# Performance work log

Hardware: AMD Instinct MI355X
Metric: run time of the kernel (lower is better)

## Reference

```python
import jax, jax.numpy as jnp
import numpy as np

D_MODEL = 1024
NUM_HEADS = 16
HEAD_DIM = D_MODEL // NUM_HEADS
B, S = 2, 2048


def setup_inputs() -> dict:
    key = jax.random.key(0)
    ks = jax.random.split(key, 8)
    scale = 1.0 / np.sqrt(D_MODEL)
    inp = {
        "query": jax.random.normal(ks[0], (B, S, D_MODEL), jnp.float32),
        "key": jax.random.normal(ks[1], (B, S, D_MODEL), jnp.float32),
        "value": jax.random.normal(ks[2], (B, S, D_MODEL), jnp.float32),
        # causal mask, broadcastable over batch and heads
        "mask": jnp.tril(jnp.ones((S, S), dtype=bool))[None, None, :, :],
        # torch nn.Linear weights: y = x @ W.T (+ b)
        "Wq": jax.random.normal(ks[3], (D_MODEL, D_MODEL), jnp.float32) * scale,
        "Wk": jax.random.normal(ks[4], (D_MODEL, D_MODEL), jnp.float32) * scale,
        "Wv": jax.random.normal(ks[5], (D_MODEL, D_MODEL), jnp.float32) * scale,
        "Wo": jax.random.normal(ks[6], (D_MODEL, D_MODEL), jnp.float32) * scale,
        "bo": jax.random.normal(ks[7], (D_MODEL,), jnp.float32) * scale,
    }
    return inp


def _split_heads(x):
    b, s, _ = x.shape
    return x.reshape(b, s, NUM_HEADS, HEAD_DIM).transpose(0, 2, 1, 3)  # [B,H,S,Dh]


def reference(query, key, value, mask, Wq, Wk, Wv, Wo, bo):
    q = _split_heads(query @ Wq.T)
    k = _split_heads(key @ Wk.T)
    v = _split_heads(value @ Wv.T)
    scores = jnp.einsum("bhqd,bhkd->bhqk", q, k) / jnp.sqrt(jnp.float32(HEAD_DIM))
    scores = jnp.where(mask, scores, jnp.float32(-jnp.inf))
    attn = jax.nn.softmax(scores, axis=-1)
    out = jnp.einsum("bhqk,bhkd->bhqd", attn, v)  # [B,H,S,Dh]
    out = out.transpose(0, 2, 1, 3).reshape(query.shape[0], q.shape[2], D_MODEL)
    return out @ Wo.T + bo
```

## Files before the change

kernel.cpp:

```cpp
#include <hip/hip_runtime.h>
#include <hip/hip_bf16.h>

#define DM   1024
#define NH   16
#define HD   64
#define SEQ  2048
#define BATCH 2
#define MTOT (BATCH*SEQ)

typedef unsigned short u16;
typedef __attribute__((ext_vector_type(8))) short bf16x8;
typedef __attribute__((ext_vector_type(4))) float f32x4;

#define SC2F 0.1803368801111464f

__device__ __forceinline__ float bf2f(u16 h) {
  union { unsigned int i; float f; } u; u.i = ((unsigned int)h) << 16; return u.f;
}
__device__ __forceinline__ u16 f2bf(float f) {
  union { float f; unsigned int i; } u; u.f = f;
  unsigned int r = u.i + 0x7fffu + ((u.i >> 16) & 1u);
  return (u16)(r >> 16);
}
__device__ __forceinline__ unsigned int pk2(float lo, float hi) {
  union { float f; unsigned int u; } a, b; a.f = lo; b.f = hi;
  return ((a.u + 0x8000u) >> 16) | ((b.u + 0x8000u) & 0xFFFF0000u);
}
__device__ __forceinline__ unsigned int cvtpk(float lo, float hi) {
  unsigned int r;
  asm("v_cvt_pk_bf16_f32 %0, %1, %2" : "=v"(r) : "v"(lo), "v"(hi));
  return r;
}

__device__ __forceinline__ uint4 load8_bf16(const void* base, size_t elemOff, bool isf32) {
  if (!isf32) return *(const uint4*)((const u16*)base + elemOff);
  const float* f = (const float*)base + elemOff;
  f32x4 a = *(const f32x4*)f;
  f32x4 b = *(const f32x4*)(f + 4);
  union { u16 h[8]; uint4 v; } r;
  r.h[0]=f2bf(a[0]); r.h[1]=f2bf(a[1]); r.h[2]=f2bf(a[2]); r.h[3]=f2bf(a[3]);
  r.h[4]=f2bf(b[0]); r.h[5]=f2bf(b[1]); r.h[6]=f2bf(b[2]); r.h[7]=f2bf(b[3]);
  return r.v;
}

__global__ __launch_bounds__(256) void prep(
    const void* __restrict__ q, const void* __restrict__ k, const void* __restrict__ v,
    const void* __restrict__ wq, const void* __restrict__ wk, const void* __restrict__ wv,
    const void* __restrict__ wo, const void* __restrict__ bo,
    u16* __restrict__ Xq, u16* __restrict__ Xk, u16* __restrict__ Xv,
    u16* __restrict__ Wqb, u16* __restrict__ Wkb, u16* __restrict__ Wvb, u16* __restrict__ Wob,
    float* __restrict__ biasf, int* __restrict__ flag_out)
{
  const int tid = threadIdx.x;
  __shared__ int cnts[4];
  {
    const u16* qs = (const u16*)q;
    int e0 = (qs[tid*2]   >> 7) & 0xFF;
    int e1 = (qs[tid*2+1] >> 7) & 0xFF;
    int c = ((e0 >= 0x6E && e0 <= 0x8F) ? 1 : 0) + ((e1 >= 0x6E && e1 <= 0x8F) ? 1 : 0);
    c += __shfl_xor(c, 1);  c += __shfl_xor(c, 2);  c += __shfl_xor(c, 4);
    c += __shfl_xor(c, 8);  c += __shfl_xor(c, 16); c += __shfl_xor(c, 32);
    if ((tid & 63) == 0) cnts[tid >> 6] = c;
  }
  __syncthreads();
  const bool isf32 = (cnts[0] + cnts[1] + cnts[2] + cnts[3]) < 400;

  const int z = blockIdx.z;
  if (z == 7) {
    if (blockIdx.x == 0) {
      if (tid == 0) *flag_out = isf32 ? 0 : 1;
      for (int i = tid; i < DM; i += 256)
        biasf[i] = isf32 ? ((const float*)bo)[i] : bf2f(((const u16*)bo)[i]);
    }
    return;
  }
  const void* src; u16* dst; size_t n;
  switch (z) {
    case 0: src=q;  dst=Xq;  n=(size_t)MTOT*DM; break;
    case 1: src=k;  dst=Xk;  n=(size_t)MTOT*DM; break;
    case 2: src=v;  dst=Xv;  n=(size_t)MTOT*DM; break;
    case 3: src=wq; dst=Wqb; n=(size_t)DM*DM;   break;
    case 4: src=wk; dst=Wkb; n=(size_t)DM*DM;   break;
    case 5: src=wv; dst=Wvb; n=(size_t)DM*DM;   break;
    default: src=wo; dst=Wob; n=(size_t)DM*DM;  break;
  }
  const size_t stride = (size_t)gridDim.x * 256 * 8;
  for (size_t i = ((size_t)blockIdx.x * 256 + tid) * 8; i < n; i += stride)
    *(uint4*)(dst + i) = load8_bf16(src, i, isf32);
}

__device__ __forceinline__ void gld16(const u16* g, u16* l) {
  __builtin_amdgcn_global_load_lds(
      (const __attribute__((address_space(1))) void*)g,
      (__attribute__((address_space(3))) void*)l, 16, 0, 0);
}

__global__ __launch_bounds__(256) void gemm_qkv(
    const u16* __restrict__ X0, const u16* __restrict__ X1, const u16* __restrict__ X2,
    const u16* __restrict__ W0, const u16* __restrict__ W1, const u16* __restrict__ W2,
    u16* __restrict__ F0, u16* __restrict__ F1, u16* __restrict__ F2)
{
  __shared__ __align__(16) u16 smem[24576];
  u16* const A0 = smem;
  u16* const A1 = smem + 4096;
  u16* const A2 = smem + 8192;
  u16* const B0 = smem + 12288;
  u16* const B1 = smem + 16384;
  u16* const B2 = smem + 20480;

  const int zz = blockIdx.z;
  const u16* X = (zz==0) ? X0 : ((zz==1) ? X1 : X2);
  const u16* W = (zz==0) ? W0 : ((zz==1) ? W1 : W2);
  u16* outF    = (zz==0) ? F0 : ((zz==1) ? F1 : F2);

  const int tid = threadIdx.x;
  const int wave = tid >> 6, lane = tid & 63, quad = lane >> 4, l16 = lane & 15;
  const int wr = wave >> 1, wc = wave & 1;
  const int m0 = blockIdx.x * 128, n0 = blockIdx.y * 128;

  const int sg = ((lane & 3) ^ ((lane >> 3) & 3)) * 8;
  const int rS = wave*32 + (lane >> 2);
  const u16* gA0 = X + (size_t)(m0 + rS)*DM + sg;
  const u16* gA1 = X + (size_t)(m0 + rS + 16)*DM + sg;
  const u16* gB0 = W + (size_t)(n0 + rS)*DM + sg;
  const u16* gB1 = W + (size_t)(n0 + rS + 16)*DM + sg;
  const int so = wave*1024;

  const int xslot8 = (quad ^ ((l16 >> 1) & 3)) * 8;

  f32x4 acc[4][4];
#pragma unroll
  for (int i = 0; i < 4; i++)
#pragma unroll
    for (int j = 0; j < 4; j++) { acc[i][j][0]=0.f; acc[i][j][1]=0.f; acc[i][j][2]=0.f; acc[i][j][3]=0.f; }

  gld16(gA0, A0 + so);
  gld16(gA1, A0 + so + 512);
  gld16(gB0, B0 + so);
  gld16(gB1, B0 + so + 512);
  asm volatile("" ::: "memory");

  int cur = 0;
  for (int k0 = 0; k0 < DM; k0 += 32) {
    u16* const Ab = (cur == 0) ? A0 : ((cur == 1) ? A1 : A2);
    u16* const Bb = (cur == 0) ? B0 : ((cur == 1) ? B1 : B2);
    const int nxt = (cur == 2) ? 0 : cur + 1;
    if (k0 + 32 < DM) {
      u16* const An = (nxt == 0) ? A0 : ((nxt == 1) ? A1 : A2);
      u16* const Bn = (nxt == 0) ? B0 : ((nxt == 1) ? B1 : B2);
      gld16(gA0 + k0 + 32, An + so);
      gld16(gA1 + k0 + 32, An + so + 512);
      gld16(gB0 + k0 + 32, Bn + so);
      gld16(gB1 + k0 + 32, Bn + so + 512);
      asm volatile("s_waitcnt vmcnt(4)" ::: "memory");
    } else {
      asm volatile("s_waitcnt vmcnt(0)" ::: "memory");
    }
    __builtin_amdgcn_s_barrier();
    asm volatile("" ::: "memory");

    bf16x8 af[4], bfr[4];
#pragma unroll
    for (int fr = 0; fr < 4; fr++)
      af[fr] = *(const bf16x8*)&Ab[(wr*64 + fr*16 + l16)*32 + xslot8];
#pragma unroll
    for (int fc = 0; fc < 4; fc++)
      bfr[fc] = *(const bf16x8*)&Bb[(wc*64 + fc*16 + l16)*32 + xslot8];
#pragma unroll
    for (int fr = 0; fr < 4; fr++)
#pragma unroll
      for (int fc = 0; fc < 4; fc++)
        acc[fr][fc] = __builtin_amdgcn_mfma_f32_16x16x32_bf16(af[fr], bfr[fc], acc[fr][fc], 0, 0, 0);

    asm volatile("" ::: "memory");
    cur = nxt;
  }

  if (zz == 2) {
    u16* const Ts = smem;
    const int bb = m0 >> 11;
    const int s0 = m0 & (SEQ-1);
#pragma unroll
    for (int p = 0; p < 2; p++) {
      __syncthreads();
      if (wc == p) {
#pragma unroll
        for (int fr = 0; fr < 4; fr++) {
#pragma unroll
          for (int fc = 0; fc < 4; fc++) {
            const int dl = fc*16 + l16;
            const int sb = wr*64 + fr*16 + quad*4;
            const int slot = (sb >> 3) ^ (dl & 15);
            u16* rowp = &Ts[dl*128 + slot*8 + (sb & 7)];
            *(unsigned int*)(rowp)     = pk2(acc[fr][fc][0], acc[fr][fc][1]);
            *(unsigned int*)(rowp + 2) = pk2(acc[fr][fc][2], acc[fr][fc][3]);
          }
        }
      }
      __syncthreads();
      const int dl2 = tid >> 2, ch4 = tid & 3;
      const int hh = (n0 + p*64) >> 6;
      u16* dst = outF + ((size_t)(bb*NH + hh)*HD + dl2)*SEQ + s0 + ch4*32;
#pragma unroll
      for (int j = 0; j < 4; j++) {
        const int c  = ch4*4 + j;
        const int lo = (c >> 2)*32 + (c & 3)*4;
        const int hi = lo + 16;
        uint2 lo2 = *(const uint2*)&Ts[dl2*128 + (((lo >> 3) ^ (dl2 & 15))*8) + (lo & 7)];
        uint2 hi2 = *(const uint2*)&Ts[dl2*128 + (((hi >> 3) ^ (dl2 & 15))*8) + (hi & 7)];
        uint4 o; o.x = lo2.x; o.y = lo2.y; o.z = hi2.x; o.w = hi2.y;
        *(uint4*)&dst[j*8] = o;
      }
    }
    return;
  }

#pragma unroll
  for (int fr = 0; fr < 4; fr++) {
#pragma unroll
    for (int rr = 0; rr < 4; rr++) {
      const int m = m0 + wr*64 + fr*16 + quad*4 + rr;
#pragma unroll
      for (int fc = 0; fc < 4; fc++) {
        const int n = n0 + wc*64 + fc*16 + l16;
        float vv = acc[fr][fc][rr];
        if (zz == 0) vv *= SC2F;
        const int b = m >> 11, s = m & (SEQ-1), h = n >> 6, d = n & (HD-1);
        outF[((size_t)(b*NH + h)*SEQ + s)*HD + d] = f2bf(vv);
      }
    }
  }
}

__global__ __launch_bounds__(256) void gemm_out(
    const u16* __restrict__ X, const u16* __restrict__ W,
    const float* __restrict__ biasf, void* __restrict__ outP,
    const int* __restrict__ dflag)
{
  __shared__ __align__(16) u16 smem[18432];
  u16* const A0 = smem;
  u16* const A1 = smem + 4096;
  u16* const A2 = smem + 8192;
  u16* const B0 = smem + 12288;
  u16* const B1 = smem + 14336;
  u16* const B2 = smem + 16384;

  const int tid = threadIdx.x;
  const int wave = tid >> 6, lane = tid & 63, quad = lane >> 4, l16 = lane & 15;
  const int wr = wave >> 1, wc = wave & 1;
  const int m0 = blockIdx.x * 128, n0 = blockIdx.y * 64;

  const int sg = ((lane & 3) ^ ((lane >> 3) & 3)) * 8;
  const int rA = wave*32 + (lane >> 2);
  const int rB = wave*16 + (lane >> 2);
  const u16* gA0 = X + (size_t)(m0 + rA)*DM + sg;
  const u16* gA1 = X + (size_t)(m0 + rA + 16)*DM + sg;
  const u16* gB0 = W + (size_t)(n0 + rB)*DM + sg;
  const int soA = wave*1024, soB = wave*512;

  const int xslot8 = (quad ^ ((l16 >> 1) & 3)) * 8;

  f32x4 acc[4][2];
#pragma unroll
  for (int i = 0; i < 4; i++)
#pragma unroll
    for (int j = 0; j < 2; j++) { acc[i][j][0]=0.f; acc[i][j][1]=0.f; acc[i][j][2]=0.f; acc[i][j][3]=0.f; }

  gld16(gA0, A0 + soA);
  gld16(gA1, A0 + soA + 512);
  gld16(gB0, B0 + soB);
  asm volatile("" ::: "memory");

  int cur = 0;
  for (int k0 = 0; k0 < DM; k0 += 32) {
    u16* const Ab = (cur == 0) ? A0 : ((cur == 1) ? A1 : A2);
    u16* const Bb = (cur == 0) ? B0 : ((cur == 1) ? B1 : B2);
    const int nxt = (cur == 2) ? 0 : cur + 1;
    if (k0 + 32 < DM) {
      u16* const An = (nxt == 0) ? A0 : ((nxt == 1) ? A1 : A2);
      u16* const Bn = (nxt == 0) ? B0 : ((nxt == 1) ? B1 : B2);
      gld16(gA0 + k0 + 32, An + soA);
      gld16(gA1 + k0 + 32, An + soA + 512);
      gld16(gB0 + k0 + 32, Bn + soB);
      asm volatile("s_waitcnt vmcnt(3)" ::: "memory");
    } else {
      asm volatile("s_waitcnt vmcnt(0)" ::: "memory");
    }
    __builtin_amdgcn_s_barrier();
    asm volatile("" ::: "memory");

    bf16x8 af[4], bfr[2];
#pragma unroll
    for (int fr = 0; fr < 4; fr++)
      af[fr] = *(const bf16x8*)&Ab[(wr*64 + fr*16 + l16)*32 + xslot8];
#pragma unroll
    for (int fc = 0; fc < 2; fc++)
      bfr[fc] = *(const bf16x8*)&Bb[(wc*32 + fc*16 + l16)*32 + xslot8];
#pragma unroll
    for (int fr = 0; fr < 4; fr++)
#pragma unroll
      for (int fc = 0; fc < 2; fc++)
        acc[fr][fc] = __builtin_amdgcn_mfma_f32_16x16x32_bf16(af[fr], bfr[fc], acc[fr][fc], 0, 0, 0);

    asm volatile("" ::: "memory");
    cur = nxt;
  }

  const bool isf32 = (*dflag == 0);
#pragma unroll
  for (int fr = 0; fr < 4; fr++) {
#pragma unroll
    for (int rr = 0; rr < 4; rr++) {
      const int m = m0 + wr*64 + fr*16 + quad*4 + rr;
#pragma unroll
      for (int fc = 0; fc < 2; fc++) {
        const int n = n0 + wc*32 + fc*16 + l16;
        float vv = acc[fr][fc][rr] + biasf[n];
        if (isf32) ((float*)outP)[(size_t)m*DM + n] = vv;
        else       ((u16*)outP)[(size_t)m*DM + n]   = f2bf(vv);
      }
    }
  }
}

__global__ __launch_bounds__(256) void attn_mfma(
    const u16* __restrict__ Qb, const u16* __restrict__ Kb,
    const u16* __restrict__ Vtb,
    u16* __restrict__ aO)
{
  __shared__ u16 Ks[2][64*64];
  __shared__ u16 Vs[2][64*64];

  const int bh = blockIdx.x;
  const int py = blockIdx.y;
  int qt;
  if      (py < 8)  qt = 31 - py;
  else if (py < 16) qt = py - 8;
  else if (py < 24) qt = 39 - py;
  else              qt = py - 16;

  const u16* Qp = Qb  + (size_t)bh * SEQ * HD;
  const u16* Kp = Kb  + (size_t)bh * SEQ * HD;
  const u16* Vp = Vtb + (size_t)bh * HD * SEQ;

  const int tid  = threadIdx.x;
  const int wave = tid >> 6, lane = tid & 63, quad = lane >> 4, l16 = lane & 15;

  const int i0 = wave*128 + lane, i1 = i0 + 64;
  const int r0 = i0 >> 3, c0 = (i0 & 7) ^ (r0 & 7);
  const int r1 = i1 >> 3, c1 = (i1 & 7) ^ (r1 & 7);
  const int kq_off0 = r0*HD + c0*8;
  const int kq_off1 = r1*HD + c1*8;
  const int v_off0  = r0*SEQ + c0*8;
  const int v_off1  = r1*SEQ + c1*8;

  const int l7 = l16 & 7;
  const int ql = wave*16 + l16;
  const int so = wave*1024;

  const int khi = qt + 1;
  const int qg = qt*64 + ql;

  const u16* qrow = Qp + (size_t)qg * HD;
  const bf16x8 bq0 = *(const bf16x8*)(qrow + quad*8);
  const bf16x8 bq1 = *(const bf16x8*)(qrow + 32 + quad*8);

  f32x4 O[4];
#pragma unroll
  for (int u = 0; u < 4; u++) { O[u][0]=0.f; O[u][1]=0.f; O[u][2]=0.f; O[u][3]=0.f; }
  float mi = -__builtin_inff();
  f32x4 lv = {0.f, 0.f, 0.f, 0.f};

  gld16(Kp + kq_off0, &Ks[0][so]);
  gld16(Kp + kq_off1, &Ks[0][so + 512]);
  gld16(Vp + v_off0, &Vs[0][so]);
  gld16(Vp + v_off1, &Vs[0][so + 512]);
  asm volatile("" ::: "memory");

  for (int kt = 0; kt < khi; kt++) {
    const int cb = kt & 1;
    const u16* kb = &Ks[cb][0];
    const u16* vb = &Vs[cb][0];
    if (kt + 1 < khi) {
      u16* kn = &Ks[cb ^ 1][so];
      u16* vn = &Vs[cb ^ 1][so];
      gld16(Kp + (kt+1)*(64*HD) + kq_off0, kn);
      gld16(Kp + (kt+1)*(64*HD) + kq_off1, kn + 512);
      gld16(Vp + (kt+1)*64 + v_off0, vn);
      gld16(Vp + (kt+1)*64 + v_off1, vn + 512);
      asm volatile("s_waitcnt vmcnt(4)" ::: "memory");
    } else {
      asm volatile("s_waitcnt vmcnt(0)" ::: "memory");
    }
    __builtin_amdgcn_s_barrier();
    asm volatile("" ::: "memory");

    f32x4 st[4];
#pragma unroll
    for (int t = 0; t < 4; t++) { st[t][0]=0.f; st[t][1]=0.f; st[t][2]=0.f; st[t][3]=0.f; }
#pragma unroll
    for (int s = 0; s < 2; s++) {
      const bf16x8 bq = s ? bq1 : bq0;
      const int ch = s*4 + quad;
#pragma unroll
      for (int t = 0; t < 4; t++) {
        bf16x8 ak = *(const bf16x8*)&kb[((t*16 + l16)*8 + (ch ^ l7))*8];
        st[t] = __builtin_amdgcn_mfma_f32_16x16x32_bf16(ak, bq, st[t], 0, 0, 0);
      }
    }

    if (kt == qt) {
#pragma unroll
      for (int t = 0; t < 4; t++)
#pragma unroll
        for (int r = 0; r < 4; r++)
          if (kt*64 + t*16 + quad*4 + r > qg) st[t][r] = -__builtin_inff();
    }

    f32x4 m01 = __builtin_elementwise_max(st[0], st[1]);
    f32x4 m23 = __builtin_elementwise_max(st[2], st[3]);
    f32x4 mm  = __builtin_elementwise_max(m01, m23);
    float mx = fmaxf(fmaxf(mm[0], mm[1]), fmaxf(mm[2], mm[3]));
    mx = fmaxf(mx, __shfl_xor(mx, 16));
    mx = fmaxf(mx, __shfl_xor(mx, 32));

    if (__any(mx > mi + 8.0f)) {
      const float nm = fmaxf(mi, mx);
      const float al = exp2f(mi - nm);
      mi = nm;
      const f32x4 alv = {al, al, al, al};
      lv *= alv;
      O[0] *= alv; O[1] *= alv; O[2] *= alv; O[3] *= alv;
    }

    const f32x4 miv = {mi, mi, mi, mi};
    unsigned int w[4][2];
    f32x4 e0, e1, e2, e3;
    {
      f32x4 d0 = st[0] - miv, d1 = st[1] - miv, d2 = st[2] - miv, d3 = st[3] - miv;
      e0[0]=exp2f(d0[0]); e0[1]=exp2f(d0[1]); e0[2]=exp2f(d0[2]); e0[3]=exp2f(d0[3]);
      e1[0]=exp2f(d1[0]); e1[1]=exp2f(d1[1]); e1[2]=exp2f(d1[2]); e1[3]=exp2f(d1[3]);
      e2[0]=exp2f(d2[0]); e2[1]=exp2f(d2[1]); e2[2]=exp2f(d2[2]); e2[3]=exp2f(d2[3]);
      e3[0]=exp2f(d3[0]); e3[1]=exp2f(d3[1]); e3[2]=exp2f(d3[2]); e3[3]=exp2f(d3[3]);
    }
    w[0][0] = cvtpk(e0[0], e0[1]); w[0][1] = cvtpk(e0[2], e0[3]);
    w[1][0] = cvtpk(e1[0], e1[1]); w[1][1] = cvtpk(e1[2], e1[3]);
    w[2][0] = cvtpk(e2[0], e2[1]); w[2][1] = cvtpk(e2[2], e2[3]);
    w[3][0] = cvtpk(e3[0], e3[1]); w[3][1] = cvtpk(e3[2], e3[3]);
    lv += (e0 + e1) + (e2 + e3);

#pragma unroll
    for (int s = 0; s < 2; s++) {
      union { unsigned int u[4]; bf16x8 v; } bp;
      bp.u[0] = w[2*s][0];   bp.u[1] = w[2*s][1];
      bp.u[2] = w[2*s+1][0]; bp.u[3] = w[2*s+1][1];
      const int ch = s*4 + quad;
#pragma unroll
      for (int u = 0; u < 4; u++) {
        bf16x8 av = *(const bf16x8*)&vb[((u*16 + l16)*8 + (ch ^ l7))*8];
        O[u] = __builtin_amdgcn_mfma_f32_16x16x32_bf16(av, bp.v, O[u], 0, 0, 0);
      }
    }

    asm volatile("" ::: "memory");
    __builtin_amdgcn_s_barrier();
    asm volatile("" ::: "memory");
  }

  float ls = (lv[0] + lv[1]) + (lv[2] + lv[3]);
  ls += __shfl_xor(ls, 16);
  ls += __shfl_xor(ls, 32);
  const float inv = 1.0f / ls;

  const int b = bh >> 4, h = bh & 15;
  u16* outp = aO + ((size_t)(b*SEQ + qt*64 + ql))*DM + h*HD;
#pragma unroll
  for (int u = 0; u < 4; u++) {
    uint2 u2;
    u2.x = pk2(O[u][0]*inv, O[u][1]*inv);
    u2.y = pk2(O[u][2]*inv, O[u][3]*inv);
    *(uint2*)&outp[u*16 + quad*4] = u2;
  }
}

extern "C" void kernel_launch(void* const* d_in, const int* in_sizes, int n_in,
                              void* d_out, int out_size, void* d_ws, size_t ws_size,
                              hipStream_t stream) {
  const void* q  = d_in[0];
  const void* k  = d_in[1];
  const void* v  = d_in[2];
  const void* wq = d_in[4];
  const void* wk = d_in[5];
  const void* wv = d_in[6];
  const void* wo = d_in[7];
  const void* bo = d_in[8];

  const size_t TX = (size_t)MTOT*DM;
  const size_t TW = (size_t)DM*DM;
  u16* ws  = (u16*)d_ws;
  u16* Xq  = ws;
  u16* Xk  = ws + TX;
  u16* Xv  = ws + 2*TX;
  u16* Wqb = ws + 3*TX;
  u16* Wkb = Wqb + TW;
  u16* Wvb = Wqb + 2*TW;
  u16* Wob = Wqb + 3*TW;
  u16* Qw  = ws + 3*TX + 4*TW;
  u16* Kw  = Qw + TX;
  u16* Vt  = Qw + 2*TX;
  u16*   aO     = Xq;
  float* biasf  = (float*)(Qw + 3*TX);
  int*   fl     = (int*)(biasf + DM);

  dim3 blk(256);
  prep<<<dim3(512, 1, 8), blk, 0, stream>>>(q, k, v, wq, wk, wv, wo, bo,
      Xq, Xk, Xv, Wqb, Wkb, Wvb, Wob, biasf, fl);
  gemm_qkv<<<dim3(MTOT/128, DM/128, 3), blk, 0, stream>>>(
      Xq, Xk, Xv, Wqb, Wkb, Wvb, Qw, Kw, Vt);
  attn_mfma<<<dim3(BATCH*NH, 32, 1), blk, 0, stream>>>(Qw, Kw, Vt, aO);
  gemm_out<<<dim3(MTOT/128, DM/64), blk, 0, stream>>>(aO, Wob, biasf, d_out, fl);
}
```

Measured before the change: 224.9 us.

## Fuse fp32-to-bf16 conversion into GEMM loads, drop separate prep conversion pass

The prep kernel no longer converts the activations and weights to bf16 in a workspace. Instead, the QKV and output GEMMs load fp32 (or bf16) directly from global memory into registers, convert them with v_cvt_pk_bf16_f32, and store the result to LDS in a register-staged double buffer. This replaces the earlier triple-buffered async global_load_lds pipeline. It removes a full read-write pass over roughly 50MB of inputs, at the cost of more VGPRs and a shallower prefetch depth in the GEMMs. In gemm_out only the weight operand is staged through registers.

```diff
diff --git a/kernel.cpp b/kernel.cpp
--- a/kernel.cpp
+++ b/kernel.cpp
@@ -31,24 +31,15 @@
   asm("v_cvt_pk_bf16_f32 %0, %1, %2" : "=v"(r) : "v"(lo), "v"(hi));
   return r;
 }
-
-__device__ __forceinline__ uint4 load8_bf16(const void* base, size_t elemOff, bool isf32) {
-  if (!isf32) return *(const uint4*)((const u16*)base + elemOff);
-  const float* f = (const float*)base + elemOff;
-  f32x4 a = *(const f32x4*)f;
-  f32x4 b = *(const f32x4*)(f + 4);
-  union { u16 h[8]; uint4 v; } r;
-  r.h[0]=f2bf(a[0]); r.h[1]=f2bf(a[1]); r.h[2]=f2bf(a[2]); r.h[3]=f2bf(a[3]);
-  r.h[4]=f2bf(b[0]); r.h[5]=f2bf(b[1]); r.h[6]=f2bf(b[2]); r.h[7]=f2bf(b[3]);
-  return r.v;
+__device__ __forceinline__ uint4 cvt8(const f32x4& a, const f32x4& b) {
+  uint4 r;
+  r.x = cvtpk(a[0], a[1]); r.y = cvtpk(a[2], a[3]);
+  r.z = cvtpk(b[0], b[1]); r.w = cvtpk(b[2], b[3]);
+  return r;
 }
 
 __global__ __launch_bounds__(256) void prep(
-    const void* __restrict__ q, const void* __restrict__ k, const void* __restrict__ v,
-    const void* __restrict__ wq, const void* __restrict__ wk, const void* __restrict__ wv,
-    const void* __restrict__ wo, const void* __restrict__ bo,
-    u16* __restrict__ Xq, u16* __restrict__ Xk, u16* __restrict__ Xv,
-    u16* __restrict__ Wqb, u16* __restrict__ Wkb, u16* __restrict__ Wvb, u16* __restrict__ Wob,
+    const void* __restrict__ q, const void* __restrict__ bo,
     float* __restrict__ biasf, int* __restrict__ flag_out)
 {
   const int tid = threadIdx.x;
@@ -64,29 +55,9 @@
   }
   __syncthreads();
   const bool isf32 = (cnts[0] + cnts[1] + cnts[2] + cnts[3]) < 400;
-
-  const int z = blockIdx.z;
-  if (z == 7) {
-    if (blockIdx.x == 0) {
-      if (tid == 0) *flag_out = isf32 ? 0 : 1;
-      for (int i = tid; i < DM; i += 256)
-        biasf[i] = isf32 ? ((const float*)bo)[i] : bf2f(((const u16*)bo)[i]);
-    }
-    return;
-  }
-  const void* src; u16* dst; size_t n;
-  switch (z) {
-    case 0: src=q;  dst=Xq;  n=(size_t)MTOT*DM; break;
-    case 1: src=k;  dst=Xk;  n=(size_t)MTOT*DM; break;
-    case 2: src=v;  dst=Xv;  n=(size_t)MTOT*DM; break;
-    case 3: src=wq; dst=Wqb; n=(size_t)DM*DM;   break;
-    case 4: src=wk; dst=Wkb; n=(size_t)DM*DM;   break;
-    case 5: src=wv; dst=Wvb; n=(size_t)DM*DM;   break;
-    default: src=wo; dst=Wob; n=(size_t)DM*DM;  break;
-  }
-  const size_t stride = (size_t)gridDim.x * 256 * 8;
-  for (size_t i = ((size_t)blockIdx.x * 256 + tid) * 8; i < n; i += stride)
-    *(uint4*)(dst + i) = load8_bf16(src, i, isf32);
+  if (tid == 0) *flag_out = isf32 ? 0 : 1;
+  for (int i = tid; i < DM; i += 256)
+    biasf[i] = isf32 ? ((const float*)bo)[i] : bf2f(((const u16*)bo)[i]);
 }
 
 __device__ __forceinline__ void gld16(const u16* g, u16* l) {
@@ -96,22 +67,23 @@
 }
 
 __global__ __launch_bounds__(256) void gemm_qkv(
-    const u16* __restrict__ X0, const u16* __restrict__ X1, const u16* __restrict__ X2,
-    const u16* __restrict__ W0, const u16* __restrict__ W1, const u16* __restrict__ W2,
-    u16* __restrict__ F0, u16* __restrict__ F1, u16* __restrict__ F2)
+    const void* __restrict__ X0, const void* __restrict__ X1, const void* __restrict__ X2,
+    const void* __restrict__ W0, const void* __restrict__ W1, const void* __restrict__ W2,
+    u16* __restrict__ F0, u16* __restrict__ F1, u16* __restrict__ F2,
+    const int* __restrict__ dflag)
 {
-  __shared__ __align__(16) u16 smem[24576];
+  __shared__ __align__(16) u16 smem[16384];
   u16* const A0 = smem;
   u16* const A1 = smem + 4096;
-  u16* const A2 = smem + 8192;
-  u16* const B0 = smem + 12288;
-  u16* const B1 = smem + 16384;
-  u16* const B2 = smem + 20480;
+  u16* const B0 = smem + 8192;
+  u16* const B1 = smem + 12288;
 
   const int zz = blockIdx.z;
-  const u16* X = (zz==0) ? X0 : ((zz==1) ? X1 : X2);
-  const u16* W = (zz==0) ? W0 : ((zz==1) ? W1 : W2);
-  u16* outF    = (zz==0) ? F0 : ((zz==1) ? F1 : F2);
+  const void* X = (zz==0) ? X0 : ((zz==1) ? X1 : X2);
+  const void* W = (zz==0) ? W0 : ((zz==1) ? W1 : W2);
+  u16* outF     = (zz==0) ? F0 : ((zz==1) ? F1 : F2);
+
+  const bool isf32 = (*dflag == 0);
 
   const int tid = threadIdx.x;
   const int wave = tid >> 6, lane = tid & 63, quad = lane >> 4, l16 = lane & 15;
@@ -120,11 +92,11 @@
 
   const int sg = ((lane & 3) ^ ((lane >> 3) & 3)) * 8;
   const int rS = wave*32 + (lane >> 2);
-  const u16* gA0 = X + (size_t)(m0 + rS)*DM + sg;
-  const u16* gA1 = X + (size_t)(m0 + rS + 16)*DM + sg;
-  const u16* gB0 = W + (size_t)(n0 + rS)*DM + sg;
-  const u16* gB1 = W + (size_t)(n0 + rS + 16)*DM + sg;
-  const int so = wave*1024;
+  const size_t offA0 = (size_t)(m0 + rS)*DM + sg;
+  const size_t offA1 = offA0 + (size_t)16*DM;
+  const size_t offB0 = (size_t)(n0 + rS)*DM + sg;
+  const size_t offB1 = offB0 + (size_t)16*DM;
+  const int wsl = wave*1024 + lane*8;
 
   const int xslot8 = (quad ^ ((l16 >> 1) & 3)) * 8;
 
@@ -134,47 +106,77 @@
 #pragma unroll
     for (int j = 0; j < 4; j++) { acc[i][j][0]=0.f; acc[i][j][1]=0.f; acc[i][j][2]=0.f; acc[i][j][3]=0.f; }
 
-  gld16(gA0, A0 + so);
-  gld16(gA1, A0 + so + 512);
-  gld16(gB0, B0 + so);
-  gld16(gB1, B0 + so + 512);
+  f32x4 fA0a, fA0b, fA1a, fA1b, fB0a, fB0b, fB1a, fB1b;
+  uint4 hA0, hA1, hB0, hB1;
+
+#define LD8(base, off)                                             \
+  if (isf32) { const float* fp = (const float*)(base) + (off);     \
+    f_a = *(const f32x4*)fp; f_b = *(const f32x4*)(fp + 4); }      \
+  else h_ = *(const uint4*)((const u16*)(base) + (off));
+
+  {
+#define LDI(base, off, fa, fb, hh) { f32x4 f_a, f_b; uint4 h_;     \
+    LD8(base, off); fa = f_a; fb = f_b; hh = h_; }
+    LDI(X, offA0, fA0a, fA0b, hA0)
+    LDI(X, offA1, fA1a, fA1b, hA1)
+    LDI(W, offB0, fB0a, fB0b, hB0)
+    LDI(W, offB1, fB1a, fB1b, hB1)
+    uint4 wA0 = isf32 ? cvt8(fA0a, fA0b) : hA0;
+    uint4 wA1 = isf32 ? cvt8(fA1a, fA1b) : hA1;
+    uint4 wB0 = isf32 ? cvt8(fB0a, fB0b) : hB0;
+    uint4 wB1 = isf32 ? cvt8(fB1a, fB1b) : hB1;
+    *(uint4*)&A0[wsl]       = wA0;
+    *(uint4*)&A0[wsl + 512] = wA1;
+    *(uint4*)&B0[wsl]       = wB0;
+    *(uint4*)&B0[wsl + 512] = wB1;
+  }
+  asm volatile("s_waitcnt lgkmcnt(0)" ::: "memory");
+  __builtin_amdgcn_s_barrier();
   asm volatile("" ::: "memory");
 
   int cur = 0;
   for (int k0 = 0; k0 < DM; k0 += 32) {
-    u16* const Ab = (cur == 0) ? A0 : ((cur == 1) ? A1 : A2);
-    u16* const Bb = (cur == 0) ? B0 : ((cur == 1) ? B1 : B2);
-    const int nxt = (cur == 2) ? 0 : cur + 1;
-    if (k0 + 32 < DM) {
-      u16* const An = (nxt == 0) ? A0 : ((nxt == 1) ? A1 : A2);
-      u16* const Bn = (nxt == 0) ? B0 : ((nxt == 1) ? B1 : B2);
-      gld16(gA0 + k0 + 32, An + so);
-      gld16(gA1 + k0 + 32, An + so + 512);
-      gld16(gB0 + k0 + 32, Bn + so);
-      gld16(gB1 + k0 + 32, Bn + so + 512);
-      asm volatile("s_waitcnt vmcnt(4)" ::: "memory");
-    } else {
-      asm volatile("s_waitcnt vmcnt(0)" ::: "memory");
+    const bool more = (k0 + 32 < DM);
+    if (more) {
+      LDI(X, offA0 + k0 + 32, fA0a, fA0b, hA0)
+      LDI(X, offA1 + k0 + 32, fA1a, fA1b, hA1)
+      LDI(W, offB0 + k0 + 32, fB0a, fB0b, hB0)
+      LDI(W, offB1 + k0 + 32, fB1a, fB1b, hB1)
+    }
+
+    u16* const Ab = cur ? A1 : A0;
+    u16* const Bb = cur ? B1 : B0;
+    bf16x8 af[4], bfr[4];
+#pragma unroll
+    for (int fr = 0; fr < 4; fr++)
+      af[fr] = *(const bf16x8*)&Ab[(wr*64 + fr*16 + l16)*32 + xslot8];
+#pragma unroll
+    for (int fc = 0; fc < 4; fc++)
+      bfr[fc] = *(const bf16x8*)&Bb[(wc*64 + fc*16 + l16)*32 + xslot8];
+#pragma unroll
+    for (int fr = 0; fr < 4; fr++)
+#pragma unroll
+      for (int fc = 0; fc < 4; fc++)
+        acc[fr][fc] = __builtin_amdgcn_mfma_f32_16x16x32_bf16(af[fr], bfr[fc], acc[fr][fc], 0, 0, 0);
+
+    if (more) {
+      u16* const An = cur ? A0 : A1;
+      u16* const Bn = cur ? B0 : B1;
+      uint4 wA0 = isf32 ? cvt8(fA0a, fA0b) : hA0;
+      uint4 wA1 = isf32 ? cvt8(fA1a, fA1b) : hA1;
+      uint4 wB0 = isf32 ? cvt8(fB0a, fB0b) : hB0;
+      uint4 wB1 = isf32 ? cvt8(fB1a, fB1b) : hB1;
+      *(uint4*)&An[wsl]       = wA0;
+      *(uint4*)&An[wsl + 512] = wA1;
+      *(uint4*)&Bn[wsl]       = wB0;
+      *(uint4*)&Bn[wsl + 512] = wB1;
+      asm volatile("s_waitcnt lgkmcnt(0)" ::: "memory");
     }
     __builtin_amdgcn_s_barrier();
     asm volatile("" ::: "memory");
-
-    bf16x8 af[4], bfr[4];
-#pragma unroll
-    for (int fr = 0; fr < 4; fr++)
-      af[fr] = *(const bf16x8*)&Ab[(wr*64 + fr*16 + l16)*32 + xslot8];
-#pragma unroll
-    for (int fc = 0; fc < 4; fc++)
-      bfr[fc] = *(const bf16x8*)&Bb[(wc*64 + fc*16 + l16)*32 + xslot8];
-#pragma unroll
-    for (int fr = 0; fr < 4; fr++)
-#pragma unroll
-      for (int fc = 0; fc < 4; fc++)
-        acc[fr][fc] = __builtin_amdgcn_mfma_f32_16x16x32_bf16(af[fr], bfr[fc], acc[fr][fc], 0, 0, 0);
-
-    asm volatile("" ::: "memory");
-    cur = nxt;
-  }
+    cur ^= 1;
+  }
+#undef LDI
 
   if (zz == 2) {
     u16* const Ts = smem;
@@ -233,17 +235,17 @@
 }
 
 __global__ __launch_bounds__(256) void gemm_out(
-    const u16* __restrict__ X, const u16* __restrict__ W,
+    const u16* __restrict__ X, const void* __restrict__ W,
     const float* __restrict__ biasf, void* __restrict__ outP,
     const int* __restrict__ dflag)
 {
-  __shared__ __align__(16) u16 smem[18432];
+  __shared__ __align__(16) u16 smem[12288];
   u16* const A0 = smem;
   u16* const A1 = smem + 4096;
-  u16* const A2 = smem + 8192;
-  u16* const B0 = smem + 12288;
-  u16* const B1 = smem + 14336;
-  u16* const B2 = smem + 16384;
+  u16* const B0 = smem + 8192;
+  u16* const B1 = smem + 10240;
+
+  const bool isf32 = (*dflag == 0);
 
   const int tid = threadIdx.x;
   const int wave = tid >> 6, lane = tid & 63, quad = lane >> 4, l16 = lane & 15;
@@ -255,8 +257,9 @@
   const int rB = wave*16 + (lane >> 2);
   const u16* gA0 = X + (size_t)(m0 + rA)*DM + sg;
   const u16* gA1 = X + (size_t)(m0 + rA + 16)*DM + sg;
-  const u16* gB0 = W + (size_t)(n0 + rB)*DM + sg;
-  const int soA = wave*1024, soB = wave*512;
+  const size_t offB = (size_t)(n0 + rB)*DM + sg;
+  const int soA = wave*1024;
+  const int wslB = wave*512 + lane*8;
 
   const int xslot8 = (quad ^ ((l16 >> 1) & 3)) * 8;
 
@@ -265,48 +268,61 @@
   for (int i = 0; i < 4; i++)
 #pragma unroll
     for (int j = 0; j < 2; j++) { acc[i][j][0]=0.f; acc[i][j][1]=0.f; acc[i][j][2]=0.f; acc[i][j][3]=0.f; }
+
+  f32x4 fBa, fBb; uint4 hB;
 
   gld16(gA0, A0 + soA);
   gld16(gA1, A0 + soA + 512);
-  gld16(gB0, B0 + soB);
+  { f32x4 f_a, f_b; uint4 h_;
+    LD8(W, offB)
+    fBa = f_a; fBb = f_b; hB = h_; }
+  {
+    uint4 wB = isf32 ? cvt8(fBa, fBb) : hB;
+    *(uint4*)&B0[wslB] = wB;
+  }
+  asm volatile("s_waitcnt vmcnt(0) lgkmcnt(0)" ::: "memory");
+  __builtin_amdgcn_s_barrier();
   asm volatile("" ::: "memory");
 
   int cur = 0;
   for (int k0 = 0; k0 < DM; k0 += 32) {
-    u16* const Ab = (cur == 0) ? A0 : ((cur == 1) ? A1 : A2);
-    u16* const Bb = (cur == 0) ? B0 : ((cur == 1) ? B1 : B2);
-    const int nxt = (cur == 2) ? 0 : cur + 1;
-    if (k0 + 32 < DM) {
-      u16* const An = (nxt == 0) ? A0 : ((nxt == 1) ? A1 : A2);
-      u16* const Bn = (nxt == 0) ? B0 : ((nxt == 1) ? B1 : B2);
+    const bool more = (k0 + 32 < DM);
+    if (more) {
+      u16* const An = cur ? A0 : A1;
       gld16(gA0 + k0 + 32, An + soA);
       gld16(gA1 + k0 + 32, An + soA + 512);
-      gld16(gB0 + k0 + 32, Bn + soB);
-      asm volatile("s_waitcnt vmcnt(3)" ::: "memory");
-    } else {
-      asm volatile("s_waitcnt vmcnt(0)" ::: "memory");
-    }
+      { f32x4 f_a, f_b; uint4 h_;
+        LD8(W, offB + k0 + 32)
+        fBa = f_a; fBb = f_b; hB = h_; }
+    }
+
+    u16* const Ab = cur ? A1 : A0;
+    u16* const Bb = cur ? B1 : B0;
+    bf16x8 af[4], bfr[2];
+#pragma unroll
+    for (int fr = 0; fr < 4; fr++)
+      af[fr] = *(const bf16x8*)&Ab[(wr*64 + fr*16 + l16)*32 + xslot8];
+#pragma unroll
+    for (int fc = 0; fc < 2; fc++)
+      bfr[fc] = *(const bf16x8*)&Bb[(wc*32 + fc*16 + l16)*32 + xslot8];
+#pragma unroll
+    for (int fr = 0; fr < 4; fr++)
+#pragma unroll
+      for (int fc = 0; fc < 2; fc++)
+        acc[fr][fc] = __builtin_amdgcn_mfma_f32_16x16x32_bf16(af[fr], bfr[fc], acc[fr][fc], 0, 0, 0);
+
+    if (more) {
+      u16* const Bn = cur ? B0 : B1;
+      uint4 wB = isf32 ? cvt8(fBa, fBb) : hB;
+      *(uint4*)&Bn[wslB] = wB;
+    }
+    asm volatile("s_waitcnt vmcnt(0) lgkmcnt(0)" ::: "memory");
     __builtin_amdgcn_s_barrier();
     asm volatile("" ::: "memory");
-
-    bf16x8 af[4], bfr[2];
-#pragma unroll
-    for (int fr = 0; fr < 4; fr++)
-      af[fr] = *(const bf16x8*)&Ab[(wr*64 + fr*16 + l16)*32 + xslot8];
-#pragma unroll
-    for (int fc = 0; fc < 2; fc++)
-      bfr[fc] = *(const bf16x8*)&Bb[(wc*32 + fc*16 + l16)*32 + xslot8];
-#pragma unroll
-    for (int fr = 0; fr < 4; fr++)
-#pragma unroll
-      for (int fc = 0; fc < 2; fc++)
-        acc[fr][fc] = __builtin_amdgcn_mfma_f32_16x16x32_bf16(af[fr], bfr[fc], acc[fr][fc], 0, 0, 0);
-
-    asm volatile("" ::: "memory");
-    cur = nxt;
-  }
-
-  const bool isf32 = (*dflag == 0);
+    cur ^= 1;
+  }
+
+  const bool isf32o = isf32;
 #pragma unroll
   for (int fr = 0; fr < 4; fr++) {
 #pragma unroll
@@ -316,8 +332,8 @@
       for (int fc = 0; fc < 2; fc++) {
         const int n = n0 + wc*32 + fc*16 + l16;
         float vv = acc[fr][fc][rr] + biasf[n];
-        if (isf32) ((float*)outP)[(size_t)m*DM + n] = vv;
-        else       ((u16*)outP)[(size_t)m*DM + n]   = f2bf(vv);
+        if (isf32o) ((float*)outP)[(size_t)m*DM + n] = vv;
+        else        ((u16*)outP)[(size_t)m*DM + n]   = f2bf(vv);
       }
     }
   }
@@ -496,27 +512,18 @@
   const void* bo = d_in[8];
 
   const size_t TX = (size_t)MTOT*DM;
-  const size_t TW = (size_t)DM*DM;
   u16* ws  = (u16*)d_ws;
-  u16* Xq  = ws;
-  u16* Xk  = ws + TX;
-  u16* Xv  = ws + 2*TX;
-  u16* Wqb = ws + 3*TX;
-  u16* Wkb = Wqb + TW;
-  u16* Wvb = Wqb + 2*TW;
-  u16* Wob = Wqb + 3*TW;
-  u16* Qw  = ws + 3*TX + 4*TW;
-  u16* Kw  = Qw + TX;
-  u16* Vt  = Qw + 2*TX;
-  u16*   aO     = Xq;
-  float* biasf  = (float*)(Qw + 3*TX);
-  int*   fl     = (int*)(biasf + DM);
+  u16* aO  = ws;
+  u16* Qw  = ws + TX;
+  u16* Kw  = ws + 2*TX;
+  u16* Vt  = ws + 3*TX;
+  float* biasf = (float*)(ws + 4*TX);
+  int*   fl    = (int*)(biasf + DM);
 
   dim3 blk(256);
-  prep<<<dim3(512, 1, 8), blk, 0, stream>>>(q, k, v, wq, wk, wv, wo, bo,
-      Xq, Xk, Xv, Wqb, Wkb, Wvb, Wob, biasf, fl);
+  prep<<<dim3(1), blk, 0, stream>>>(q, bo, biasf, fl);
   gemm_qkv<<<dim3(MTOT/128, DM/128, 3), blk, 0, stream>>>(
-      Xq, Xk, Xv, Wqb, Wkb, Wvb, Qw, Kw, Vt);
+      q, k, v, wq, wk, wv, Qw, Kw, Vt, fl);
   attn_mfma<<<dim3(BATCH*NH, 32, 1), blk, 0, stream>>>(Qw, Kw, Vt, aO);
-  gemm_out<<<dim3(MTOT/128, DM/64), blk, 0, stream>>>(aO, Wob, biasf, d_out, fl);
-}
+  gemm_out<<<dim3(MTOT/128, DM/64), blk, 0, stream>>>(aO, wo, biasf, d_out, fl);
+}
```

New measurement: 312.0 us. 1.39x slower.

## Fuse fp32-to-bf16 activation conversion into QKV GEMM A-tile loads

Applied to the files above, without the earlier changes.

The prep kernel no longer converts the three large q/k/v activation tensors to bf16. The QKV GEMM now reads the raw inputs through registers, converts them with v_cvt_pk_bf16_f32 and writes them to LDS, with the pipeline changed from three to two LDS buffers. This removes a full read and write pass over the activations, at the cost of register-staged A loads that can no longer use direct global-to-LDS copies. Conversion is repeated for each N tile, and the rounding differs slightly from the old f2bf.

```diff
diff --git a/kernel.cpp b/kernel.cpp
--- a/kernel.cpp
+++ b/kernel.cpp
@@ -29,6 +29,12 @@
 __device__ __forceinline__ unsigned int cvtpk(float lo, float hi) {
   unsigned int r;
   asm("v_cvt_pk_bf16_f32 %0, %1, %2" : "=v"(r) : "v"(lo), "v"(hi));
+  return r;
+}
+__device__ __forceinline__ uint4 cvt8(const f32x4& a, const f32x4& b) {
+  uint4 r;
+  r.x = cvtpk(a[0], a[1]); r.y = cvtpk(a[2], a[3]);
+  r.z = cvtpk(b[0], b[1]); r.w = cvtpk(b[2], b[3]);
   return r;
 }
 
@@ -44,11 +50,12 @@
 }
 
 __global__ __launch_bounds__(256) void prep(
-    const void* __restrict__ q, const void* __restrict__ k, const void* __restrict__ v,
-    const void* __restrict__ wq, const void* __restrict__ wk, const void* __restrict__ wv,
-    const void* __restrict__ wo, const void* __restrict__ bo,
-    u16* __restrict__ Xq, u16* __restrict__ Xk, u16* __restrict__ Xv,
-    u16* __restrict__ Wqb, u16* __restrict__ Wkb, u16* __restrict__ Wvb, u16* __restrict__ Wob,
+    const void* __restrict__ q,
+    const void* __restrict__ wq, const void* __restrict__ wk,
+    const void* __restrict__ wv, const void* __restrict__ wo,
+    const void* __restrict__ bo,
+    u16* __restrict__ Wqb, u16* __restrict__ Wkb,
+    u16* __restrict__ Wvb, u16* __restrict__ Wob,
     float* __restrict__ biasf, int* __restrict__ flag_out)
 {
   const int tid = threadIdx.x;
@@ -66,7 +73,7 @@
   const bool isf32 = (cnts[0] + cnts[1] + cnts[2] + cnts[3]) < 400;
 
   const int z = blockIdx.z;
-  if (z == 7) {
+  if (z == 4) {
     if (blockIdx.x == 0) {
       if (tid == 0) *flag_out = isf32 ? 0 : 1;
       for (int i = tid; i < DM; i += 256)
@@ -74,16 +81,9 @@
     }
     return;
   }
-  const void* src; u16* dst; size_t n;
-  switch (z) {
-    case 0: src=q;  dst=Xq;  n=(size_t)MTOT*DM; break;
-    case 1: src=k;  dst=Xk;  n=(size_t)MTOT*DM; break;
-    case 2: src=v;  dst=Xv;  n=(size_t)MTOT*DM; break;
-    case 3: src=wq; dst=Wqb; n=(size_t)DM*DM;   break;
-    case 4: src=wk; dst=Wkb; n=(size_t)DM*DM;   break;
-    case 5: src=wv; dst=Wvb; n=(size_t)DM*DM;   break;
-    default: src=wo; dst=Wob; n=(size_t)DM*DM;  break;
-  }
+  const void* src = (z==0) ? wq : (z==1) ? wk : (z==2) ? wv : wo;
+  u16* dst        = (z==0) ? Wqb : (z==1) ? Wkb : (z==2) ? Wvb : Wob;
+  const size_t n = (size_t)DM*DM;
   const size_t stride = (size_t)gridDim.x * 256 * 8;
   for (size_t i = ((size_t)blockIdx.x * 256 + tid) * 8; i < n; i += stride)
     *(uint4*)(dst + i) = load8_bf16(src, i, isf32);
@@ -96,22 +96,23 @@
 }
 
 __global__ __launch_bounds__(256) void gemm_qkv(
-    const u16* __restrict__ X0, const u16* __restrict__ X1, const u16* __restrict__ X2,
+    const void* __restrict__ X0, const void* __restrict__ X1, const void* __restrict__ X2,
     const u16* __restrict__ W0, const u16* __restrict__ W1, const u16* __restrict__ W2,
-    u16* __restrict__ F0, u16* __restrict__ F1, u16* __restrict__ F2)
+    u16* __restrict__ F0, u16* __restrict__ F1, u16* __restrict__ F2,
+    const int* __restrict__ dflag)
 {
-  __shared__ __align__(16) u16 smem[24576];
+  __shared__ __align__(16) u16 smem[16384];
   u16* const A0 = smem;
   u16* const A1 = smem + 4096;
-  u16* const A2 = smem + 8192;
-  u16* const B0 = smem + 12288;
-  u16* const B1 = smem + 16384;
-  u16* const B2 = smem + 20480;
+  u16* const B0 = smem + 8192;
+  u16* const B1 = smem + 12288;
 
   const int zz = blockIdx.z;
-  const u16* X = (zz==0) ? X0 : ((zz==1) ? X1 : X2);
-  const u16* W = (zz==0) ? W0 : ((zz==1) ? W1 : W2);
-  u16* outF    = (zz==0) ? F0 : ((zz==1) ? F1 : F2);
+  const void* X = (zz==0) ? X0 : ((zz==1) ? X1 : X2);
+  const u16* W  = (zz==0) ? W0 : ((zz==1) ? W1 : W2);
+  u16* outF     = (zz==0) ? F0 : ((zz==1) ? F1 : F2);
+
+  const bool isf32 = (*dflag == 0);
 
   const int tid = threadIdx.x;
   const int wave = tid >> 6, lane = tid & 63, quad = lane >> 4, l16 = lane & 15;
@@ -120,11 +121,12 @@
 
   const int sg = ((lane & 3) ^ ((lane >> 3) & 3)) * 8;
   const int rS = wave*32 + (lane >> 2);
-  const u16* gA0 = X + (size_t)(m0 + rS)*DM + sg;
-  const u16* gA1 = X + (size_t)(m0 + rS + 16)*DM + sg;
+  const size_t offA0 = (size_t)(m0 + rS)*DM + sg;
+  const size_t offA1 = offA0 + (size_t)16*DM;
   const u16* gB0 = W + (size_t)(n0 + rS)*DM + sg;
-  const u16* gB1 = W + (size_t)(n0 + rS + 16)*DM + sg;
-  const int so = wave*1024;
+  const u16* gB1 = gB0 + (size_t)16*DM;
+  const int so  = wave*1024;
+  const int wsl = wave*1024 + lane*8;
 
   const int xslot8 = (quad ^ ((l16 >> 1) & 3)) * 8;
 
@@ -134,29 +136,48 @@
 #pragma unroll
     for (int j = 0; j < 4; j++) { acc[i][j][0]=0.f; acc[i][j][1]=0.f; acc[i][j][2]=0.f; acc[i][j][3]=0.f; }
 
-  gld16(gA0, A0 + so);
-  gld16(gA1, A0 + so + 512);
+  f32x4 fa0, fb0, fa1, fb1; uint4 ha0, ha1;
+
+#define LDA(koff)                                                   \
+  if (isf32) {                                                      \
+    const float* p0 = (const float*)X + offA0 + (koff);             \
+    fa0 = *(const f32x4*)p0; fb0 = *(const f32x4*)(p0 + 4);         \
+    const float* p1 = (const float*)X + offA1 + (koff);             \
+    fa1 = *(const f32x4*)p1; fb1 = *(const f32x4*)(p1 + 4);         \
+  } else {                                                          \
+    ha0 = *(const uint4*)((const u16*)X + offA0 + (koff));          \
+    ha1 = *(const uint4*)((const u16*)X + offA1 + (koff));          \
+  }
+#define WRA(buf) {                                                  \
+    uint4 w0 = isf32 ? cvt8(fa0, fb0) : ha0;                        \
+    uint4 w1 = isf32 ? cvt8(fa1, fb1) : ha1;                        \
+    *(uint4*)&(buf)[wsl]       = w0;                                \
+    *(uint4*)&(buf)[wsl + 512] = w1;                                \
+  }
+
+  LDA(0)
   gld16(gB0, B0 + so);
   gld16(gB1, B0 + so + 512);
+  asm volatile("s_waitcnt vmcnt(0)" ::: "memory");
+  WRA(A0)
+  LDA(32)
+  asm volatile("s_waitcnt lgkmcnt(0)" ::: "memory");
+  __builtin_amdgcn_s_barrier();
   asm volatile("" ::: "memory");
 
   int cur = 0;
   for (int k0 = 0; k0 < DM; k0 += 32) {
-    u16* const Ab = (cur == 0) ? A0 : ((cur == 1) ? A1 : A2);
-    u16* const Bb = (cur == 0) ? B0 : ((cur == 1) ? B1 : B2);
-    const int nxt = (cur == 2) ? 0 : cur + 1;
-    if (k0 + 32 < DM) {
-      u16* const An = (nxt == 0) ? A0 : ((nxt == 1) ? A1 : A2);
-      u16* const Bn = (nxt == 0) ? B0 : ((nxt == 1) ? B1 : B2);
-      gld16(gA0 + k0 + 32, An + so);
-      gld16(gA1 + k0 + 32, An + so + 512);
+    u16* const Ab = cur ? A1 : A0;
+    u16* const Bb = cur ? B1 : B0;
+    u16* const An = cur ? A0 : A1;
+    u16* const Bn = cur ? B0 : B1;
+    const bool more  = (k0 + 32 < DM);
+    const bool more2 = (k0 + 64 < DM);
+
+    if (more) {
       gld16(gB0 + k0 + 32, Bn + so);
       gld16(gB1 + k0 + 32, Bn + so + 512);
-      asm volatile("s_waitcnt vmcnt(4)" ::: "memory");
-    } else {
-      asm volatile("s_waitcnt vmcnt(0)" ::: "memory");
-    }
-    __builtin_amdgcn_s_barrier();
+    }
     asm volatile("" ::: "memory");
 
     bf16x8 af[4], bfr[4];
@@ -172,9 +193,24 @@
       for (int fc = 0; fc < 4; fc++)
         acc[fr][fc] = __builtin_amdgcn_mfma_f32_16x16x32_bf16(af[fr], bfr[fc], acc[fr][fc], 0, 0, 0);
 
-    asm volatile("" ::: "memory");
-    cur = nxt;
-  }
+    if (more) {
+      asm volatile("s_waitcnt vmcnt(2)" ::: "memory");
+      WRA(An)
+      if (more2) { LDA(k0 + 64) }
+      if (more2) {
+        if (isf32) { asm volatile("s_waitcnt vmcnt(4)" ::: "memory"); }
+        else       { asm volatile("s_waitcnt vmcnt(2)" ::: "memory"); }
+      } else {
+        asm volatile("s_waitcnt vmcnt(0)" ::: "memory");
+      }
+      asm volatile("s_waitcnt lgkmcnt(0)" ::: "memory");
+    }
+    __builtin_amdgcn_s_barrier();
+    asm volatile("" ::: "memory");
+    cur ^= 1;
+  }
+#undef LDA
+#undef WRA
 
   if (zz == 2) {
     u16* const Ts = smem;
@@ -498,25 +534,22 @@
   const size_t TX = (size_t)MTOT*DM;
   const size_t TW = (size_t)DM*DM;
   u16* ws  = (u16*)d_ws;
-  u16* Xq  = ws;
-  u16* Xk  = ws + TX;
-  u16* Xv  = ws + 2*TX;
-  u16* Wqb = ws + 3*TX;
+  u16* aO  = ws;
+  u16* Qw  = ws + TX;
+  u16* Kw  = ws + 2*TX;
+  u16* Vt  = ws + 3*TX;
+  u16* Wqb = ws + 4*TX;
   u16* Wkb = Wqb + TW;
   u16* Wvb = Wqb + 2*TW;
   u16* Wob = Wqb + 3*TW;
-  u16* Qw  = ws + 3*TX + 4*TW;
-  u16* Kw  = Qw + TX;
-  u16* Vt  = Qw + 2*TX;
-  u16*   aO     = Xq;
-  float* biasf  = (float*)(Qw + 3*TX);
-  int*   fl     = (int*)(biasf + DM);
+  float* biasf = (float*)(Wqb + 4*TW);
+  int*   fl    = (int*)(biasf + DM);
 
   dim3 blk(256);
-  prep<<<dim3(512, 1, 8), blk, 0, stream>>>(q, k, v, wq, wk, wv, wo, bo,
-      Xq, Xk, Xv, Wqb, Wkb, Wvb, Wob, biasf, fl);
+  prep<<<dim3(256, 1, 5), blk, 0, stream>>>(q, wq, wk, wv, wo, bo,
+      Wqb, Wkb, Wvb, Wob, biasf, fl);
   gemm_qkv<<<dim3(MTOT/128, DM/128, 3), blk, 0, stream>>>(
-      Xq, Xk, Xv, Wqb, Wkb, Wvb, Qw, Kw, Vt);
+      q, k, v, Wqb, Wkb, Wvb, Qw, Kw, Vt, fl);
   attn_mfma<<<dim3(BATCH*NH, 32, 1), blk, 0, stream>>>(Qw, Kw, Vt, aO);
   gemm_out<<<dim3(MTOT/128, DM/64), blk, 0, stream>>>(aO, Wob, biasf, d_out, fl);
 }
```

Measured after the change: 258.6 us. 1.15x slower.
